# Kernel tuning notes

Hardware: AMD Instinct MI355X
Metric: run time of the kernel (lower is better)

The kernel has to match this reference:

```python
import jax, jax.numpy as jnp
import numpy as np

B, S, D = 4, 2048, 128


def setup_inputs() -> dict:
    key = jax.random.key(0)
    kq, kk, kv = jax.random.split(key, 3)
    query = jax.random.normal(kq, (B, S, D), dtype=jnp.float32)
    key_t = jax.random.normal(kk, (B, S, D), dtype=jnp.float32)
    value = jax.random.normal(kv, (B, S, D), dtype=jnp.float32)
    return {"query": query, "key": key_t, "value": value}


def reference(query, key, value):
    # Raw dot-general attention: contract only the last dim, NO batch dims,
    # so scores have shape [B, Sq, B, Sk] (cross-batch attention).
    scores = jnp.einsum('aqd,bkd->aqbk', query, key)  # [B,S,B,S]
    # softmax over the trailing half of the dims (axes 2 and 3 jointly)
    attn = jax.nn.softmax(scores, axis=(2, 3))
    # Dropout: train=False -> deterministic no-op.
    # Second dot_general contracts trailing (B,Sk) of attn with leading (B,Sk) of value.
    y = jnp.einsum('aqbk,bkd->aqd', attn, value)  # [B,S,D]
    return y
```

## Files before the change

### kernel.cpp

```cpp
#include <hip/hip_runtime.h>
#include <hip/hip_bf16.h>
#include <string.h>

#define NROWS 8192
#define DH    128
#define G     16
#define KPG   (NROWS / G)
#define NIT   (KPG / 32)
#define SEGS  16
#define B32U  (SEGS * 512)
#define LOG2E 1.44269504088896340736f
#define MSCALED (56.0f * LOG2E)

typedef __attribute__((ext_vector_type(8)))  short    short8;
typedef __attribute__((ext_vector_type(16))) float    floatx16;
typedef __attribute__((ext_vector_type(4)))  unsigned short us4;
typedef __attribute__((ext_vector_type(8)))  _Float16 half8;
typedef __attribute__((ext_vector_type(4)))  _Float16 half4;

#define MFMA_BF32(a, b, c)  __builtin_amdgcn_mfma_f32_32x32x16_bf16((a), (b), (c), 0, 0, 0)
#define MFMA_F16W(a, b, c)  __builtin_amdgcn_mfma_f32_32x32x16_f16((a), (b), (c), 0, 0, 0)

__device__ __forceinline__ unsigned short f32_to_bf16(float f) {
    union { float f; unsigned u; } v; v.f = f;
    unsigned u = v.u + 0x7FFFu + ((v.u >> 16) & 1u);
    return (unsigned short)(u >> 16);
}
__device__ __forceinline__ float bf16_to_f32(unsigned short h) {
    union { unsigned u; float f; } v; v.u = ((unsigned)h) << 16;
    return v.f;
}
__device__ __forceinline__ float fast_exp2(float x) {
    float r; asm("v_exp_f32 %0, %1" : "=v"(r) : "v"(x)); return r;
}
__device__ __forceinline__ void async_ld16(const void* g, void* lds) {
    __builtin_amdgcn_global_load_lds(
        (const __attribute__((address_space(1))) unsigned int*)g,
        (__attribute__((address_space(3))) unsigned int*)lds, 16, 0, 0);
}

__global__ void prep_kernel(const float* __restrict__ Q, const float* __restrict__ K,
                            const float* __restrict__ V,
                            _Float16* __restrict__ Qf, unsigned short* __restrict__ KV) {
    int bid = blockIdx.x;
    if (bid < 1024) {
        int i = bid * 1024 + threadIdx.x * 4;
        float4 q = *(const float4*)(Q + i);
        half4 o = {(_Float16)q.x, (_Float16)q.y, (_Float16)q.z, (_Float16)q.w};
        *(half4*)(Qf + i) = o;
        return;
    }
    if (bid < 1152) {
        int B = bid - 1024;
        const float* Ksrc = K + (size_t)B * 64 * DH;
        unsigned short* dst = KV + (size_t)(2 * B) * B32U;
#pragma unroll
        for (int j = 0; j < 4; j++) {
            int ch = j * 256 + threadIdx.x;
            int mt = ch >> 9;
            int rem = ch & 511;
            int c = rem >> 6;
            int within = rem & 63;
            int h = within >> 5, l31 = within & 31;
            const float* src = Ksrc + (size_t)(mt * 32 + l31) * DH + c * 16 + h * 8;
            float4 a = *(const float4*)src;
            float4 b = *(const float4*)(src + 4);
            half8 o = {(_Float16)a.x, (_Float16)a.y, (_Float16)a.z, (_Float16)a.w,
                       (_Float16)b.x, (_Float16)b.y, (_Float16)b.z, (_Float16)b.w};
            *(half8*)(dst + (size_t)mt * B32U + c * 512 + within * 8) = o;
        }
        return;
    }
    int B = bid - 1152;
    __shared__ unsigned short tile[64][132];
    const float* Vsrc = V + (size_t)B * 64 * DH;
    {
        int row = threadIdx.x >> 2;
        int cb0 = (threadIdx.x & 3) * 32;
#pragma unroll
        for (int j = 0; j < 8; j++) {
            float4 v = *(const float4*)(Vsrc + (size_t)row * DH + cb0 + j * 4);
            tile[row][cb0 + j * 4 + 0] = f32_to_bf16(v.x);
            tile[row][cb0 + j * 4 + 1] = f32_to_bf16(v.y);
            tile[row][cb0 + j * 4 + 2] = f32_to_bf16(v.z);
            tile[row][cb0 + j * 4 + 3] = f32_to_bf16(v.w);
        }
    }
    __syncthreads();
    unsigned short* dstv = KV + (size_t)(2 * B) * B32U + 8 * 512;
#pragma unroll
    for (int j = 0; j < 4; j++) {
        int ch = j * 256 + threadIdx.x;
        int mt = ch >> 9;
        int rem = ch & 511;
        int seg = rem >> 6;
        int within = rem & 63;
        int h = within >> 5, rr = within & 31;
        int t = seg >> 1, sp = seg & 1;
        int d = t * 32 + rr;
        short8 o;
#pragma unroll
        for (int jj = 0; jj < 8; jj++) {
            int p = mt * 32 + sp * 16 + h * 8 + jj;
            int ar = (p & ~12) | ((p & 8) >> 1) | ((p & 4) << 1);
            o[jj] = tile[ar][d];
        }
        *(short8*)(dstv + (size_t)mt * B32U + seg * 512 + within * 8) = o;
    }
}

__launch_bounds__(256, 4)
__global__ void attn_kernel(const _Float16* __restrict__ Qf,
                            const unsigned short* __restrict__ KV,
                            unsigned short* __restrict__ Opart,
                            float* __restrict__ lsum) {
    __shared__ __align__(16) unsigned short kvbuf[2][SEGS * 512];

    const int lane = threadIdx.x & 63;
    const int wave = threadIdx.x >> 6;
    const int g    = blockIdx.x & (G - 1);
    const int qt   = blockIdx.x / G;
    const int l31  = lane & 31;
    const int h    = lane >> 5;
    const int qrow0 = qt * 128 + wave * 32;

    half8 qf[8];
    {
        const half8* ph = (const half8*)(Qf + (size_t)(qrow0 + l31) * DH + h * 8);
#pragma unroll
        for (int c = 0; c < 8; c++) qf[c] = ph[c * 2];
    }

    floatx16 Oacc[4];
#pragma unroll
    for (int t = 0; t < 4; t++)
#pragma unroll
        for (int e = 0; e < 16; e++) Oacc[t][e] = 0.f;
    float la0 = 0.f, la1 = 0.f;

    const unsigned short* pb = KV + (size_t)(g * NIT) * B32U + lane * 8;
    auto stage = [&](int buf) {
        unsigned short* dst = kvbuf[buf];
#pragma unroll
        for (int j = 0; j < 4; j++) {
            int s = wave + 4 * j;
            async_ld16(pb + s * 512, dst + s * 512);
        }
        pb += B32U;
    };

    const int fo = lane * 8;

    stage(0);
    for (int it = 0; it < NIT; ++it) {
        __syncthreads();
        if (it + 1 < NIT) stage((it + 1) & 1);

        const unsigned short* cb = kvbuf[it & 1];

        floatx16 S;
#pragma unroll
        for (int e = 0; e < 16; e++) S[e] = 0.f;
        __builtin_amdgcn_s_setprio(1);
#pragma unroll
        for (int c = 0; c < 8; c++) {
            half8 a = *(const half8*)(cb + c * 512 + fo);
            S = MFMA_F16W(a, qf[c], S);
        }
        __builtin_amdgcn_s_setprio(0);

#pragma unroll
        for (int sp = 0; sp < 2; sp++) {
            union { unsigned u[4]; short8 s8; } bp;
            float lad = 0.f;
#pragma unroll
            for (int e = 0; e < 4; e++) {
                float pa  = fast_exp2(__builtin_fmaf(S[8 * sp + 2 * e],     LOG2E, -MSCALED));
                float pb2 = fast_exp2(__builtin_fmaf(S[8 * sp + 2 * e + 1], LOG2E, -MSCALED));
                lad += pa; lad += pb2;
                __hip_bfloat162 pk = __float22bfloat162_rn(float2{pa, pb2});
                unsigned u; memcpy(&u, &pk, 4);
                bp.u[e] = u;
            }
            if (sp == 0) la0 += lad; else la1 += lad;
            __builtin_amdgcn_s_setprio(1);
#pragma unroll
            for (int t = 0; t < 4; t++) {
                short8 vf = *(const short8*)(cb + (8 + t * 2 + sp) * 512 + fo);
                Oacc[t] = MFMA_BF32(vf, bp.s8, Oacc[t]);
            }
            __builtin_amdgcn_s_setprio(0);
        }
    }

    unsigned short* op = Opart + ((size_t)g * NROWS + qrow0 + l31) * DH;
#pragma unroll
    for (int t = 0; t < 4; t++)
#pragma unroll
        for (int rg = 0; rg < 4; rg++) {
            us4 w;
#pragma unroll
            for (int e = 0; e < 4; e++) w[e] = f32_to_bf16(Oacc[t][4 * rg + e]);
            *(us4*)(op + 32 * t + 8 * rg + 4 * h) = w;
        }
    float lacc = la0 + la1;
    lacc += __shfl_xor(lacc, 32);
    if (h == 0) lsum[(size_t)g * NROWS + qrow0 + l31] = lacc;
}

__global__ void merge_kernel(const unsigned short* __restrict__ Opart,
                             const float* __restrict__ lsum, float* __restrict__ out) {
    int t = blockIdx.x * 256 + threadIdx.x;
    int base = t * 8;
    int q = base >> 7;
    float L = 0.f;
#pragma unroll
    for (int g = 0; g < G; g++) L += lsum[(size_t)g * NROWS + q];
    float acc[8] = {0.f, 0.f, 0.f, 0.f, 0.f, 0.f, 0.f, 0.f};
#pragma unroll
    for (int g = 0; g < G; g++) {
        short8 v = *(const short8*)(Opart + (size_t)g * NROWS * DH + base);
#pragma unroll
        for (int j = 0; j < 8; j++) acc[j] += bf16_to_f32((unsigned short)v[j]);
    }
    float inv = 1.0f / L;
    float4 o0 = {acc[0] * inv, acc[1] * inv, acc[2] * inv, acc[3] * inv};
    float4 o1 = {acc[4] * inv, acc[5] * inv, acc[6] * inv, acc[7] * inv};
    *(float4*)(out + base) = o0;
    *(float4*)(out + base + 4) = o1;
}

extern "C" void kernel_launch(void* const* d_in, const int* in_sizes, int n_in,
                              void* d_out, int out_size, void* d_ws, size_t ws_size,
                              hipStream_t stream) {
    const float* Q = (const float*)d_in[0];
    const float* K = (const float*)d_in[1];
    const float* V = (const float*)d_in[2];
    float* out = (float*)d_out;

    char* ws = (char*)d_ws;
    _Float16* Qf = (_Float16*)ws;
    unsigned short* KV = (unsigned short*)(ws + (size_t)NROWS * DH * 2);
    char* p = ws + (size_t)NROWS * DH * 2 + (size_t)(NROWS / 32) * B32U * 2;
    unsigned short* Opart = (unsigned short*)p;
    float* lsum = (float*)(p + (size_t)G * NROWS * DH * sizeof(unsigned short));

    hipLaunchKernelGGL(prep_kernel, dim3(1024 + 128 + 128), dim3(256), 0, stream,
                       Q, K, V, Qf, KV);
    hipLaunchKernelGGL(attn_kernel, dim3((NROWS / 128) * G), dim3(256), 0, stream,
                       Qf, KV, Opart, lsum);
    hipLaunchKernelGGL(merge_kernel, dim3(NROWS * DH / (256 * 8)), dim3(256), 0, stream,
                       Opart, lsum, out);
}
```

Baseline: 126.6 us.

## Process two query tiles per wave and halve key-split groups

Each wave now handles 64 query rows, split into two 32-row MFMA tiles that share every K/V fragment read from LDS. Each iteration now stages 64 keys instead of 32. The key dimension is split into 8 groups instead of 16, and the grid has 256 blocks instead of 1024. This raises arithmetic intensity per LDS and global load and halves the partial outputs the merge kernel reads. In exchange, register pressure roughly doubles, launch bounds drop to one block per SM, LDS per block doubles, and there are fewer blocks to hide latency across the 256 CUs.

```diff
diff --git a/kernel.cpp b/kernel.cpp
--- a/kernel.cpp
+++ b/kernel.cpp
@@ -4,11 +4,10 @@
 
 #define NROWS 8192
 #define DH    128
-#define G     16
+#define G     8
 #define KPG   (NROWS / G)
-#define NIT   (KPG / 32)
-#define SEGS  16
-#define B32U  (SEGS * 512)
+#define NIT   (KPG / 64)
+#define B32U  (16 * 512)
 #define LOG2E 1.44269504088896340736f
 #define MSCALED (56.0f * LOG2E)
 
@@ -109,12 +108,12 @@
     }
 }
 
-__launch_bounds__(256, 4)
+__launch_bounds__(256, 1)
 __global__ void attn_kernel(const _Float16* __restrict__ Qf,
                             const unsigned short* __restrict__ KV,
                             unsigned short* __restrict__ Opart,
                             float* __restrict__ lsum) {
-    __shared__ __align__(16) unsigned short kvbuf[2][SEGS * 512];
+    __shared__ __align__(16) unsigned short kvbuf[2][32 * 512];
 
     const int lane = threadIdx.x & 63;
     const int wave = threadIdx.x >> 6;
@@ -122,31 +121,32 @@
     const int qt   = blockIdx.x / G;
     const int l31  = lane & 31;
     const int h    = lane >> 5;
-    const int qrow0 = qt * 128 + wave * 32;
-
-    half8 qf[8];
+    const int qrow0 = qt * 256 + wave * 64;
+
+    half8 qfA[8], qfB[8];
     {
-        const half8* ph = (const half8*)(Qf + (size_t)(qrow0 + l31) * DH + h * 8);
-#pragma unroll
-        for (int c = 0; c < 8; c++) qf[c] = ph[c * 2];
-    }
-
-    floatx16 Oacc[4];
+        const half8* pa = (const half8*)(Qf + (size_t)(qrow0 + l31) * DH + h * 8);
+        const half8* pbq = (const half8*)(Qf + (size_t)(qrow0 + 32 + l31) * DH + h * 8);
+#pragma unroll
+        for (int c = 0; c < 8; c++) { qfA[c] = pa[c * 2]; qfB[c] = pbq[c * 2]; }
+    }
+
+    floatx16 OaccA[4], OaccB[4];
 #pragma unroll
     for (int t = 0; t < 4; t++)
 #pragma unroll
-        for (int e = 0; e < 16; e++) Oacc[t][e] = 0.f;
-    float la0 = 0.f, la1 = 0.f;
-
-    const unsigned short* pb = KV + (size_t)(g * NIT) * B32U + lane * 8;
+        for (int e = 0; e < 16; e++) { OaccA[t][e] = 0.f; OaccB[t][e] = 0.f; }
+    float laA = 0.f, laB = 0.f;
+
+    const unsigned short* pb = KV + (size_t)(g * (KPG / 32)) * B32U + lane * 8;
     auto stage = [&](int buf) {
         unsigned short* dst = kvbuf[buf];
 #pragma unroll
-        for (int j = 0; j < 4; j++) {
+        for (int j = 0; j < 8; j++) {
             int s = wave + 4 * j;
             async_ld16(pb + s * 512, dst + s * 512);
         }
-        pb += B32U;
+        pb += 2 * B32U;
     };
 
     const int fo = lane * 8;
@@ -158,54 +158,74 @@
 
         const unsigned short* cb = kvbuf[it & 1];
 
-        floatx16 S;
-#pragma unroll
-        for (int e = 0; e < 16; e++) S[e] = 0.f;
-        __builtin_amdgcn_s_setprio(1);
-#pragma unroll
-        for (int c = 0; c < 8; c++) {
-            half8 a = *(const half8*)(cb + c * 512 + fo);
-            S = MFMA_F16W(a, qf[c], S);
-        }
-        __builtin_amdgcn_s_setprio(0);
-
-#pragma unroll
-        for (int sp = 0; sp < 2; sp++) {
-            union { unsigned u[4]; short8 s8; } bp;
-            float lad = 0.f;
-#pragma unroll
-            for (int e = 0; e < 4; e++) {
-                float pa  = fast_exp2(__builtin_fmaf(S[8 * sp + 2 * e],     LOG2E, -MSCALED));
-                float pb2 = fast_exp2(__builtin_fmaf(S[8 * sp + 2 * e + 1], LOG2E, -MSCALED));
-                lad += pa; lad += pb2;
-                __hip_bfloat162 pk = __float22bfloat162_rn(float2{pa, pb2});
-                unsigned u; memcpy(&u, &pk, 4);
-                bp.u[e] = u;
-            }
-            if (sp == 0) la0 += lad; else la1 += lad;
+#pragma unroll
+        for (int mt = 0; mt < 2; mt++) {
+            const unsigned short* cm = cb + mt * B32U;
+
+            floatx16 S0, S1;
+#pragma unroll
+            for (int e = 0; e < 16; e++) { S0[e] = 0.f; S1[e] = 0.f; }
             __builtin_amdgcn_s_setprio(1);
 #pragma unroll
-            for (int t = 0; t < 4; t++) {
-                short8 vf = *(const short8*)(cb + (8 + t * 2 + sp) * 512 + fo);
-                Oacc[t] = MFMA_BF32(vf, bp.s8, Oacc[t]);
+            for (int c = 0; c < 8; c++) {
+                half8 a = *(const half8*)(cm + c * 512 + fo);
+                S0 = MFMA_F16W(a, qfA[c], S0);
+                S1 = MFMA_F16W(a, qfB[c], S1);
             }
             __builtin_amdgcn_s_setprio(0);
-        }
-    }
-
-    unsigned short* op = Opart + ((size_t)g * NROWS + qrow0 + l31) * DH;
+
+#pragma unroll
+            for (int sp = 0; sp < 2; sp++) {
+                union { unsigned u[4]; short8 s8; } bpA, bpB;
+                float ladA = 0.f, ladB = 0.f;
+#pragma unroll
+                for (int e = 0; e < 4; e++) {
+                    float a0 = fast_exp2(__builtin_fmaf(S0[8 * sp + 2 * e],     LOG2E, -MSCALED));
+                    float a1 = fast_exp2(__builtin_fmaf(S0[8 * sp + 2 * e + 1], LOG2E, -MSCALED));
+                    float b0 = fast_exp2(__builtin_fmaf(S1[8 * sp + 2 * e],     LOG2E, -MSCALED));
+                    float b1 = fast_exp2(__builtin_fmaf(S1[8 * sp + 2 * e + 1], LOG2E, -MSCALED));
+                    ladA += a0; ladA += a1;
+                    ladB += b0; ladB += b1;
+                    __hip_bfloat162 pkA = __float22bfloat162_rn(float2{a0, a1});
+                    __hip_bfloat162 pkB = __float22bfloat162_rn(float2{b0, b1});
+                    unsigned uA, uB;
+                    memcpy(&uA, &pkA, 4); memcpy(&uB, &pkB, 4);
+                    bpA.u[e] = uA; bpB.u[e] = uB;
+                }
+                laA += ladA; laB += ladB;
+                __builtin_amdgcn_s_setprio(1);
+#pragma unroll
+                for (int t = 0; t < 4; t++) {
+                    short8 vf = *(const short8*)(cm + (8 + t * 2 + sp) * 512 + fo);
+                    OaccA[t] = MFMA_BF32(vf, bpA.s8, OaccA[t]);
+                    OaccB[t] = MFMA_BF32(vf, bpB.s8, OaccB[t]);
+                }
+                __builtin_amdgcn_s_setprio(0);
+            }
+        }
+    }
+
+    unsigned short* opA = Opart + ((size_t)g * NROWS + qrow0 + l31) * DH;
+    unsigned short* opB = Opart + ((size_t)g * NROWS + qrow0 + 32 + l31) * DH;
 #pragma unroll
     for (int t = 0; t < 4; t++)
 #pragma unroll
         for (int rg = 0; rg < 4; rg++) {
-            us4 w;
-#pragma unroll
-            for (int e = 0; e < 4; e++) w[e] = f32_to_bf16(Oacc[t][4 * rg + e]);
-            *(us4*)(op + 32 * t + 8 * rg + 4 * h) = w;
-        }
-    float lacc = la0 + la1;
-    lacc += __shfl_xor(lacc, 32);
-    if (h == 0) lsum[(size_t)g * NROWS + qrow0 + l31] = lacc;
+            us4 wA, wB;
+#pragma unroll
+            for (int e = 0; e < 4; e++) {
+                wA[e] = f32_to_bf16(OaccA[t][4 * rg + e]);
+                wB[e] = f32_to_bf16(OaccB[t][4 * rg + e]);
+            }
+            *(us4*)(opA + 32 * t + 8 * rg + 4 * h) = wA;
+            *(us4*)(opB + 32 * t + 8 * rg + 4 * h) = wB;
+        }
+    laA += __shfl_xor(laA, 32);
+    laB += __shfl_xor(laB, 32);
+    if (h == 0) {
+        lsum[(size_t)g * NROWS + qrow0 + l31] = laA;
+        lsum[(size_t)g * NROWS + qrow0 + 32 + l31] = laB;
+    }
 }
 
 __global__ void merge_kernel(const unsigned short* __restrict__ Opart,
@@ -247,7 +267,7 @@
 
     hipLaunchKernelGGL(prep_kernel, dim3(1024 + 128 + 128), dim3(256), 0, stream,
                        Q, K, V, Qf, KV);
-    hipLaunchKernelGGL(attn_kernel, dim3((NROWS / 128) * G), dim3(256), 0, stream,
+    hipLaunchKernelGGL(attn_kernel, dim3((NROWS / 256) * G), dim3(256), 0, stream,
                        Qf, KV, Opart, lsum);
     hipLaunchKernelGGL(merge_kernel, dim3(NROWS * DH / (256 * 8)), dim3(256), 0, stream,
                        Opart, lsum, out);
```

After: 116.8 us. 1.08x faster.

## Process two key blocks per iteration and halve split-K groups

Applied to the files above, without the earlier changes.

Each iteration now stages and processes 64 keys (two 32-key blocks) instead of 32. Two independent score accumulators are computed, exponentiated and fed to the PV MFMAs, which raises instruction-level parallelism and halves barrier count per key. The split-K group count drops from 16 to 8, halving partial outputs written and merged. In exchange, LDS per block doubles, register pressure rises, occupancy bound drops to 2 blocks per CU, and the grid shrinks.

```diff
diff --git a/kernel.cpp b/kernel.cpp
--- a/kernel.cpp
+++ b/kernel.cpp
@@ -4,11 +4,10 @@
 
 #define NROWS 8192
 #define DH    128
-#define G     16
+#define G     8
 #define KPG   (NROWS / G)
-#define NIT   (KPG / 32)
-#define SEGS  16
-#define B32U  (SEGS * 512)
+#define NIT   (KPG / 64)
+#define B32U  (16 * 512)
 #define LOG2E 1.44269504088896340736f
 #define MSCALED (56.0f * LOG2E)
 
@@ -109,17 +108,17 @@
     }
 }
 
-__launch_bounds__(256, 4)
+__launch_bounds__(256, 2)
 __global__ void attn_kernel(const _Float16* __restrict__ Qf,
                             const unsigned short* __restrict__ KV,
                             unsigned short* __restrict__ Opart,
                             float* __restrict__ lsum) {
-    __shared__ __align__(16) unsigned short kvbuf[2][SEGS * 512];
+    __shared__ __align__(16) unsigned short kvbuf[2][32 * 512];
 
     const int lane = threadIdx.x & 63;
     const int wave = threadIdx.x >> 6;
     const int g    = blockIdx.x & (G - 1);
-    const int qt   = blockIdx.x / G;
+    const int qt   = blockIdx.x >> 3;
     const int l31  = lane & 31;
     const int h    = lane >> 5;
     const int qrow0 = qt * 128 + wave * 32;
@@ -136,17 +135,17 @@
     for (int t = 0; t < 4; t++)
 #pragma unroll
         for (int e = 0; e < 16; e++) Oacc[t][e] = 0.f;
-    float la0 = 0.f, la1 = 0.f;
-
-    const unsigned short* pb = KV + (size_t)(g * NIT) * B32U + lane * 8;
+    float lacc = 0.f;
+
+    const unsigned short* pb = KV + (size_t)(g * (KPG / 32)) * B32U + lane * 8;
     auto stage = [&](int buf) {
         unsigned short* dst = kvbuf[buf];
 #pragma unroll
-        for (int j = 0; j < 4; j++) {
+        for (int j = 0; j < 8; j++) {
             int s = wave + 4 * j;
             async_ld16(pb + s * 512, dst + s * 512);
         }
-        pb += B32U;
+        pb += 2 * B32U;
     };
 
     const int fo = lane * 8;
@@ -158,39 +157,52 @@
 
         const unsigned short* cb = kvbuf[it & 1];
 
-        floatx16 S;
-#pragma unroll
-        for (int e = 0; e < 16; e++) S[e] = 0.f;
+        floatx16 S0, S1;
+#pragma unroll
+        for (int e = 0; e < 16; e++) { S0[e] = 0.f; S1[e] = 0.f; }
         __builtin_amdgcn_s_setprio(1);
 #pragma unroll
         for (int c = 0; c < 8; c++) {
-            half8 a = *(const half8*)(cb + c * 512 + fo);
-            S = MFMA_F16W(a, qf[c], S);
+            half8 a0 = *(const half8*)(cb + c * 512 + fo);
+            half8 a1 = *(const half8*)(cb + (16 + c) * 512 + fo);
+            S0 = MFMA_F16W(a0, qf[c], S0);
+            S1 = MFMA_F16W(a1, qf[c], S1);
         }
         __builtin_amdgcn_s_setprio(0);
 
-#pragma unroll
-        for (int sp = 0; sp < 2; sp++) {
-            union { unsigned u[4]; short8 s8; } bp;
-            float lad = 0.f;
-#pragma unroll
-            for (int e = 0; e < 4; e++) {
-                float pa  = fast_exp2(__builtin_fmaf(S[8 * sp + 2 * e],     LOG2E, -MSCALED));
-                float pb2 = fast_exp2(__builtin_fmaf(S[8 * sp + 2 * e + 1], LOG2E, -MSCALED));
-                lad += pa; lad += pb2;
-                __hip_bfloat162 pk = __float22bfloat162_rn(float2{pa, pb2});
-                unsigned u; memcpy(&u, &pk, 4);
-                bp.u[e] = u;
+        short8 bp0[2], bp1[2];
+        auto expack = [&](const floatx16& S, short8 (&bp)[2]) {
+#pragma unroll
+            for (int sp = 0; sp < 2; sp++) {
+                union { unsigned u[4]; short8 s8; } pk;
+                float l0 = 0.f, l1 = 0.f;
+#pragma unroll
+                for (int e = 0; e < 4; e++) {
+                    float pa  = fast_exp2(__builtin_fmaf(S[8 * sp + 2 * e],     LOG2E, -MSCALED));
+                    float pb2 = fast_exp2(__builtin_fmaf(S[8 * sp + 2 * e + 1], LOG2E, -MSCALED));
+                    l0 += pa; l1 += pb2;
+                    __hip_bfloat162 c2 = __float22bfloat162_rn(float2{pa, pb2});
+                    unsigned u; memcpy(&u, &c2, 4);
+                    pk.u[e] = u;
+                }
+                lacc += l0 + l1;
+                bp[sp] = pk.s8;
             }
-            if (sp == 0) la0 += lad; else la1 += lad;
-            __builtin_amdgcn_s_setprio(1);
+        };
+        expack(S0, bp0);
+        expack(S1, bp1);
+
+        __builtin_amdgcn_s_setprio(1);
+#pragma unroll
+        for (int sp = 0; sp < 2; sp++)
 #pragma unroll
             for (int t = 0; t < 4; t++) {
-                short8 vf = *(const short8*)(cb + (8 + t * 2 + sp) * 512 + fo);
-                Oacc[t] = MFMA_BF32(vf, bp.s8, Oacc[t]);
+                short8 vf0 = *(const short8*)(cb + (8 + t * 2 + sp) * 512 + fo);
+                Oacc[t] = MFMA_BF32(vf0, bp0[sp], Oacc[t]);
+                short8 vf1 = *(const short8*)(cb + (16 + 8 + t * 2 + sp) * 512 + fo);
+                Oacc[t] = MFMA_BF32(vf1, bp1[sp], Oacc[t]);
             }
-            __builtin_amdgcn_s_setprio(0);
-        }
+        __builtin_amdgcn_s_setprio(0);
     }
 
     unsigned short* op = Opart + ((size_t)g * NROWS + qrow0 + l31) * DH;
@@ -203,7 +215,6 @@
             for (int e = 0; e < 4; e++) w[e] = f32_to_bf16(Oacc[t][4 * rg + e]);
             *(us4*)(op + 32 * t + 8 * rg + 4 * h) = w;
         }
-    float lacc = la0 + la1;
     lacc += __shfl_xor(lacc, 32);
     if (h == 0) lsum[(size_t)g * NROWS + qrow0 + l31] = lacc;
 }
```

Measured after the change: 113.4 us. 10.4% less time.
